# Performance work log

Measured on AMD Instinct MI355X. Metric: run time of the kernel, lower is better.

The kernel has to match this reference:

```python
import jax, jax.numpy as jnp
import numpy as np

K_NEIGHBORS = 16


def knn_idx(x, k):
    # x: (bs, n, 3) -> (bs, n, k) indices of k nearest points (incl. self)
    sq = jnp.sum(x * x, axis=-1)                      # (bs, n)
    inner = jnp.einsum('bnd,bmd->bnm', x, x)          # (bs, n, n)
    dist = sq[:, :, None] - 2.0 * inner + sq[:, None, :]
    _, idx = jax.lax.top_k(-dist, k)
    return idx


def gather_neighbors(feat, idx):
    # feat: (bs, n, d), idx: (bs, n, k) -> (bs, n, k, d)
    bs = feat.shape[0]
    return feat[jnp.arange(bs)[:, None, None], idx]


def setup_inputs() -> dict:
    key = jax.random.key(0)
    ks = jax.random.split(key, 20)
    bs, n, emb, inner, ph, ah = 4, 2048, 128, 128, 64, 4 * 128
    s = lambda k, sh, fan: jax.random.normal(k, sh, jnp.float32) * (1.0 / np.sqrt(fan))
    return {
        'query': jax.random.normal(ks[0], (bs, n, emb), jnp.float32),
        'key': jax.random.normal(ks[1], (bs, n, emb), jnp.float32),
        'value': jax.random.normal(ks[2], (bs, n, emb), jnp.float32),
        'canonical': jax.random.normal(ks[3], (bs, n, 3), jnp.float32),
        'wq': s(ks[4], (emb, inner), emb),
        'wk': s(ks[5], (emb, inner), emb),
        'wv': s(ks[6], (emb, inner), emb),
        'wo': s(ks[7], (inner, emb), inner),
        'bo': jnp.zeros((emb,), jnp.float32),
        'p1': s(ks[8], (3, ph), 3),
        'pb1': jnp.zeros((ph,), jnp.float32),
        'p2': s(ks[9], (ph, inner), ph),
        'pb2': jnp.zeros((inner,), jnp.float32),
        'a1': s(ks[10], (inner, ah), inner),
        'ab1': jnp.zeros((ah,), jnp.float32),
        'a2': s(ks[11], (ah, inner), ah),
        'ab2': jnp.zeros((inner,), jnp.float32),
    }


def reference(query, key, value, canonical, wq, wk, wv, wo, bo,
              p1, pb1, p2, pb2, a1, ab1, a2, ab2):
    k_nb = K_NEIGHBORS
    q = query @ wq                                    # (bs, n, d)
    k = key @ wk
    v = value @ wv
    idx = knn_idx(canonical, k_nb)                    # (bs, n, k)

    pos_nn = gather_neighbors(canonical, idx)         # (bs, n, k, 3)
    rel_pos = pos_nn - canonical[:, :, None, :]
    rel_pos_emb = jax.nn.relu(rel_pos @ p1 + pb1) @ p2 + pb2  # (bs, n, k, d)

    q_nn = gather_neighbors(q, idx)
    k_nn = gather_neighbors(k, idx)
    v_nn = gather_neighbors(v, idx) + rel_pos_emb

    sim = jax.nn.relu((q_nn - k_nn + rel_pos_emb) @ a1 + ab1) @ a2 + ab2
    attn = jax.nn.softmax(sim, axis=-1)               # softmax over feature dim
    norm = jnp.maximum(jnp.linalg.norm(attn, axis=-2, keepdims=True), 1e-12)
    attn = attn / norm                                # L2-normalize over neighbors

    agg = jnp.einsum('bijd,bijd->bid', attn, v_nn)    # (bs, n, d)
    return agg @ wo + bo
```

## Files before the change

kernel.cpp:

```cpp
#include <hip/hip_runtime.h>
#include <stdint.h>

typedef unsigned short u16;
typedef unsigned int u32;
typedef unsigned long long u64;
typedef __attribute__((ext_vector_type(8))) short short8;
typedef __attribute__((ext_vector_type(4))) float f32x4;

#define BSZ 4
#define NPT 2048
#define EMB 128
#define PH  64
#define AH  512
#define KNB 16

__device__ __forceinline__ u16 f2bf(float f) {
  union { float f; u32 u; } v; v.f = f;
  u32 r = (v.u >> 16) & 1u;
  v.u += 0x7fffu + r;
  return (u16)(v.u >> 16);
}
__device__ __forceinline__ float bf2f(u16 x) {
  union { u32 u; float f; } v; v.u = ((u32)x) << 16; return v.f;
}

__global__ __launch_bounds__(256) void k_transpose(
    const float* wq, const float* wk, const float* wv, const float* p2,
    const float* a1, const float* a2, const float* wo,
    u16* wqT, u16* wkT, u16* wvT, u16* p2T, u16* a1T, u16* a2T, u16* woT) {
  const float* src; u16* dst; int K, Nn;
  switch (blockIdx.x) {
    case 0: src = wq; dst = wqT; K = 128; Nn = 128; break;
    case 1: src = wk; dst = wkT; K = 128; Nn = 128; break;
    case 2: src = wv; dst = wvT; K = 128; Nn = 128; break;
    case 3: src = p2; dst = p2T; K = 64;  Nn = 128; break;
    case 4: src = a1; dst = a1T; K = 128; Nn = 512; break;
    case 5: src = a2; dst = a2T; K = 512; Nn = 128; break;
    default: src = wo; dst = woT; K = 128; Nn = 128; break;
  }
  for (int n = threadIdx.x; n < Nn; n += 256) {
    for (int k0 = 0; k0 < K; k0 += 8) {
      short8 vv;
      #pragma unroll
      for (int t = 0; t < 8; ++t)
        vv[t] = (short)f2bf(src[(k0 + t) * Nn + n]);
      *(short8*)(dst + n * K + k0) = vv;
    }
  }
}

__device__ __forceinline__ u32 f2sort(float f) {
  union { float f; u32 u; } v; v.f = f;
  return v.u ^ ((v.u >> 31) ? 0xFFFFFFFFu : 0x80000000u);
}

__global__ __launch_bounds__(256) void k_knn(const float* __restrict__ can,
                                             int* __restrict__ idx_out) {
  __shared__ float dists[4][NPT];
  int b = blockIdx.x >> 8;
  int qblk = blockIdx.x & 255;
  const float* cb = can + (size_t)b * NPT * 3;
  int wave = threadIdx.x >> 6, lane = threadIdx.x & 63;
  float* dw = dists[wave];
  #pragma unroll 1
  for (int t = 0; t < 2; ++t) {
    int i = qblk * 8 + wave * 2 + t;
    float xi = cb[i * 3 + 0], yi = cb[i * 3 + 1], zi = cb[i * 3 + 2];
    float sqi = __fadd_rn(__fadd_rn(__fmul_rn(xi, xi), __fmul_rn(yi, yi)),
                          __fmul_rn(zi, zi));
    u64 lmin = ~0ull;
    #pragma unroll 4
    for (int c = 0; c < NPT / 64; ++c) {
      int j = c * 64 + lane;
      const float* pj = cb + j * 3;
      float xj = pj[0], yj = pj[1], zj = pj[2];
      float sqj = __fadd_rn(__fadd_rn(__fmul_rn(xj, xj), __fmul_rn(yj, yj)),
                            __fmul_rn(zj, zj));
      float nn = __fadd_rn(__fadd_rn(__fmul_rn(xi, xj), __fmul_rn(yi, yj)),
                           __fmul_rn(zi, zj));
      float dist = __fadd_rn(__fsub_rn(sqi, __fmul_rn(2.0f, nn)), sqj);
      dw[j] = dist;
      u64 key = (((u64)f2sort(dist)) << 32) | (u32)j;
      lmin = key < lmin ? key : lmin;
    }
    #pragma unroll 1
    for (int r = 0; r < KNB; ++r) {
      u64 g = lmin;
      #pragma unroll
      for (int off = 32; off > 0; off >>= 1) {
        u64 o = __shfl_xor(g, off);
        g = o < g ? o : g;
      }
      int jw = (int)(u32)(g & 0xffffffffull);
      if (lane == 0) idx_out[((size_t)b * NPT + i) * KNB + r] = jw;
      if ((jw & 63) == lane) {
        union { u32 u; float f; } inf; inf.u = 0x7f800000u;
        dw[jw] = inf.f;
        lmin = ~0ull;
        #pragma unroll
        for (int c = 0; c < NPT / 64; ++c) {
          int j = c * 64 + lane;
          u64 key = (((u64)f2sort(dw[j])) << 32) | (u32)j;
          lmin = key < lmin ? key : lmin;
        }
      }
    }
  }
}

__device__ __forceinline__ void qkv_gemm(const u16* At, const u16* wT,
                                         int colbase, int fm, int quad,
                                         f32x4 acc[2][4]) {
  #pragma unroll
  for (int tn = 0; tn < 2; ++tn)
    #pragma unroll
    for (int tm = 0; tm < 4; ++tm) acc[tn][tm] = (f32x4){0.f, 0.f, 0.f, 0.f};
  #pragma unroll
  for (int ks = 0; ks < 4; ++ks) {
    int k0 = ks * 32 + quad * 8;
    short8 bfr0 = *(const short8*)(wT + (colbase + fm) * 128 + k0);
    short8 bfr1 = *(const short8*)(wT + (colbase + 16 + fm) * 128 + k0);
    #pragma unroll
    for (int tm = 0; tm < 4; ++tm) {
      short8 afr = *(const short8*)(At + (tm * 16 + fm) * 136 + k0);
      acc[0][tm] = __builtin_amdgcn_mfma_f32_16x16x32_bf16(afr, bfr0, acc[0][tm], 0, 0, 0);
      acc[1][tm] = __builtin_amdgcn_mfma_f32_16x16x32_bf16(afr, bfr1, acc[1][tm], 0, 0, 0);
    }
  }
}

__device__ __forceinline__ void qkv_stage(u16* At, const float* src, int rbase, int tid) {
  #pragma unroll
  for (int rep = 0; rep < 4; ++rep) {
    int linear = tid + 256 * rep;
    int row = linear >> 4;
    int c16 = linear & 15;
    const float* sp = src + (size_t)(rbase + row) * 128 + c16 * 8;
    f32x4 a = *(const f32x4*)(sp);
    f32x4 b = *(const f32x4*)(sp + 4);
    short8 vv;
    vv[0] = (short)f2bf(a[0]); vv[1] = (short)f2bf(a[1]);
    vv[2] = (short)f2bf(a[2]); vv[3] = (short)f2bf(a[3]);
    vv[4] = (short)f2bf(b[0]); vv[5] = (short)f2bf(b[1]);
    vv[6] = (short)f2bf(b[2]); vv[7] = (short)f2bf(b[3]);
    *(short8*)(At + row * 136 + c16 * 8) = vv;
  }
}

__global__ __launch_bounds__(256) void k_qkv(
    const float* __restrict__ query, const float* __restrict__ key,
    const float* __restrict__ value,
    const u16* __restrict__ wqT, const u16* __restrict__ wkT,
    const u16* __restrict__ wvT,
    float* __restrict__ qk_out, float* __restrict__ v_out) {
  __shared__ __align__(16) u16 At[64 * 136];
  int tid = threadIdx.x;
  int rbase = blockIdx.x * 64;
  int lane = tid & 63, wave = tid >> 6;
  int fm = lane & 15, quad = lane >> 4;
  int colbase = wave * 32;
  f32x4 accq[2][4], acck[2][4];

  qkv_stage(At, query, rbase, tid);
  __syncthreads();
  qkv_gemm(At, wqT, colbase, fm, quad, accq);
  __syncthreads();
  qkv_stage(At, key, rbase, tid);
  __syncthreads();
  qkv_gemm(At, wkT, colbase, fm, quad, acck);
  #pragma unroll
  for (int tn = 0; tn < 2; ++tn) {
    int col = colbase + tn * 16 + fm;
    #pragma unroll
    for (int tm = 0; tm < 4; ++tm)
      #pragma unroll
      for (int r = 0; r < 4; ++r) {
        int row = tm * 16 + quad * 4 + r;
        qk_out[(size_t)(rbase + row) * 128 + col] =
            accq[tn][tm][r] - acck[tn][tm][r];
      }
  }
  __syncthreads();
  qkv_stage(At, value, rbase, tid);
  __syncthreads();
  qkv_gemm(At, wvT, colbase, fm, quad, accq);
  #pragma unroll
  for (int tn = 0; tn < 2; ++tn) {
    int col = colbase + tn * 16 + fm;
    #pragma unroll
    for (int tm = 0; tm < 4; ++tm)
      #pragma unroll
      for (int r = 0; r < 4; ++r) {
        int row = tm * 16 + quad * 4 + r;
        v_out[(size_t)(rbase + row) * 128 + col] = accq[tn][tm][r];
      }
  }
}

#define XT_LD 136

__global__ __launch_bounds__(256, 3) void k_attn(
    const float* __restrict__ can,
    const float* __restrict__ qk_g, const float* __restrict__ v_g,
    const int* __restrict__ idx_g,
    const float* __restrict__ p1, const float* __restrict__ pb1,
    const u16* __restrict__ p2T, const float* __restrict__ pb2,
    const u16* __restrict__ a1T, const float* __restrict__ ab1,
    const u16* __restrict__ a2T, const float* __restrict__ ab2,
    const u16* __restrict__ woT, const float* __restrict__ bo,
    float* __restrict__ out) {
  __shared__ __align__(16) char smem[39168];
  u16* Xt = (u16*)(smem);
  u16* Hs = (u16*)(smem + 17408);
  u16* R1 = (u16*)(smem + 17408);
  float* Red1 = (float*)(smem + 34816);
  float* Red2 = (float*)(smem + 35840);
  float* Agg = (float*)(smem + 36864);
  int* Idx = (int*)(smem + 38912);

  const int b = blockIdx.x >> 9;
  const int qbase = (blockIdx.x & 511) * 4;
  const int tid = threadIdx.x;
  const int lane = tid & 63, wave = tid >> 6;
  const int fm = lane & 15, quad = lane >> 4;
  const int colbase = wave * 32;

  if (tid < 64) Idx[tid] = idx_g[((size_t)b * NPT + qbase) * KNB + tid];
  __syncthreads();

  {
    int row = tid >> 2, part = tid & 3;
    int j = Idx[row];
    int qi = qbase + (row >> 4);
    const float* cb = can + (size_t)b * NPT * 3;
    float r0 = cb[j * 3 + 0] - cb[qi * 3 + 0];
    float r1 = cb[j * 3 + 1] - cb[qi * 3 + 1];
    float r2 = cb[j * 3 + 2] - cb[qi * 3 + 2];
    #pragma unroll
    for (int hp = 0; hp < 8; ++hp) {
      int cp = part + 4 * hp;
      u32 pack = 0;
      #pragma unroll
      for (int e = 0; e < 2; ++e) {
        int hh = cp * 2 + e;
        float s = r0 * p1[hh];
        s = fmaf(r1, p1[PH + hh], s);
        s = fmaf(r2, p1[2 * PH + hh], s);
        s += pb1[hh];
        s = fmaxf(s, 0.0f);
        pack |= ((u32)f2bf(s)) << (16 * e);
      }
      *(u32*)(R1 + row * 72 + cp * 2) = pack;
    }
  }
  __syncthreads();

  u32 vp[4][4];
  {
    f32x4 acc[2][4];
    #pragma unroll
    for (int tn = 0; tn < 2; ++tn)
      #pragma unroll
      for (int tm = 0; tm < 4; ++tm) acc[tn][tm] = (f32x4){0.f, 0.f, 0.f, 0.f};
    #pragma unroll
    for (int ks = 0; ks < 2; ++ks) {
      int k0 = ks * 32 + quad * 8;
      short8 bfr0 = *(const short8*)(p2T + (colbase + fm) * PH + k0);
      short8 bfr1 = *(const short8*)(p2T + (colbase + 16 + fm) * PH + k0);
      #pragma unroll
      for (int tm = 0; tm < 4; ++tm) {
        short8 afr = *(const short8*)(R1 + (tm * 16 + fm) * 72 + k0);
        acc[0][tm] = __builtin_amdgcn_mfma_f32_16x16x32_bf16(afr, bfr0, acc[0][tm], 0, 0, 0);
        acc[1][tm] = __builtin_amdgcn_mfma_f32_16x16x32_bf16(afr, bfr1, acc[1][tm], 0, 0, 0);
      }
    }
    #pragma unroll
    for (int tn = 0; tn < 2; ++tn) {
      int col = colbase + tn * 16 + fm;
      float pb2c = pb2[col];
      #pragma unroll
      for (int tm = 0; tm < 4; ++tm)
        #pragma unroll
        for (int r = 0; r < 4; ++r) {
          int row = tm * 16 + quad * 4 + r;
          int j = Idx[row];
          float rpe = acc[tn][tm][r] + pb2c;
          size_t base = ((size_t)b * NPT + j) * EMB + col;
          Xt[row * XT_LD + col] = f2bf(qk_g[base] + rpe);
          u32 vb = (u32)f2bf(v_g[base] + rpe);
          if (tn == 0) vp[tm][r] = vb; else vp[tm][r] |= vb << 16;
        }
    }
  }
  __syncthreads();

  f32x4 accS[2][4];
  #pragma unroll
  for (int tn = 0; tn < 2; ++tn)
    #pragma unroll
    for (int tm = 0; tm < 4; ++tm) accS[tn][tm] = (f32x4){0.f, 0.f, 0.f, 0.f};
  #pragma unroll 1
  for (int c = 0; c < 4; ++c) {
    f32x4 acc1[2][4];
    #pragma unroll
    for (int tn = 0; tn < 2; ++tn)
      #pragma unroll
      for (int tm = 0; tm < 4; ++tm) acc1[tn][tm] = (f32x4){0.f, 0.f, 0.f, 0.f};
    #pragma unroll
    for (int ks = 0; ks < 4; ++ks) {
      int k0 = ks * 32 + quad * 8;
      short8 bfr0 = *(const short8*)(a1T + (c * 128 + colbase + fm) * 128 + k0);
      short8 bfr1 = *(const short8*)(a1T + (c * 128 + colbase + 16 + fm) * 128 + k0);
      #pragma unroll
      for (int tm = 0; tm < 4; ++tm) {
        short8 afr = *(const short8*)(Xt + (tm * 16 + fm) * XT_LD + k0);
        acc1[0][tm] = __builtin_amdgcn_mfma_f32_16x16x32_bf16(afr, bfr0, acc1[0][tm], 0, 0, 0);
        acc1[1][tm] = __builtin_amdgcn_mfma_f32_16x16x32_bf16(afr, bfr1, acc1[1][tm], 0, 0, 0);
      }
    }
    #pragma unroll
    for (int tn = 0; tn < 2; ++tn) {
      int lcol = colbase + tn * 16 + fm;
      float ab1c = ab1[c * 128 + lcol];
      #pragma unroll
      for (int tm = 0; tm < 4; ++tm)
        #pragma unroll
        for (int r = 0; r < 4; ++r) {
          int row = tm * 16 + quad * 4 + r;
          Hs[row * XT_LD + lcol] = f2bf(fmaxf(acc1[tn][tm][r] + ab1c, 0.0f));
        }
    }
    __syncthreads();
    #pragma unroll
    for (int ks = 0; ks < 4; ++ks) {
      int k0 = ks * 32 + quad * 8;
      short8 bfr0 = *(const short8*)(a2T + (colbase + fm) * AH + c * 128 + k0);
      short8 bfr1 = *(const short8*)(a2T + (colbase + 16 + fm) * AH + c * 128 + k0);
      #pragma unroll
      for (int tm = 0; tm < 4; ++tm) {
        short8 afr = *(const short8*)(Hs + (tm * 16 + fm) * XT_LD + k0);
        accS[0][tm] = __builtin_amdgcn_mfma_f32_16x16x32_bf16(afr, bfr0, accS[0][tm], 0, 0, 0);
        accS[1][tm] = __builtin_amdgcn_mfma_f32_16x16x32_bf16(afr, bfr1, accS[1][tm], 0, 0, 0);
      }
    }
    __syncthreads();
  }

  {
    float ab2c0 = ab2[colbase + fm];
    float ab2c1 = ab2[colbase + 16 + fm];
    float rm[4][4];
    #pragma unroll
    for (int tm = 0; tm < 4; ++tm)
      #pragma unroll
      for (int r = 0; r < 4; ++r) {
        accS[0][tm][r] += ab2c0;
        accS[1][tm][r] += ab2c1;
        rm[tm][r] = fmaxf(accS[0][tm][r], accS[1][tm][r]);
      }
    #pragma unroll
    for (int off = 1; off <= 8; off <<= 1)
      #pragma unroll
      for (int tm = 0; tm < 4; ++tm)
        #pragma unroll
        for (int r = 0; r < 4; ++r)
          rm[tm][r] = fmaxf(rm[tm][r], __shfl_xor(rm[tm][r], off));
    if (fm == 0) {
      #pragma unroll
      for (int tm = 0; tm < 4; ++tm)
        #pragma unroll
        for (int r = 0; r < 4; ++r)
          Red1[wave * 64 + tm * 16 + quad * 4 + r] = rm[tm][r];
    }
    __syncthreads();
    #pragma unroll
    for (int tm = 0; tm < 4; ++tm)
      #pragma unroll
      for (int r = 0; r < 4; ++r) {
        int row = tm * 16 + quad * 4 + r;
        float m = fmaxf(fmaxf(Red1[row], Red1[64 + row]),
                        fmaxf(Red1[128 + row], Red1[192 + row]));
        float e0 = __expf(accS[0][tm][r] - m);
        float e1 = __expf(accS[1][tm][r] - m);
        accS[0][tm][r] = e0;
        accS[1][tm][r] = e1;
        rm[tm][r] = e0 + e1;
      }
    #pragma unroll
    for (int off = 1; off <= 8; off <<= 1)
      #pragma unroll
      for (int tm = 0; tm < 4; ++tm)
        #pragma unroll
        for (int r = 0; r < 4; ++r)
          rm[tm][r] += __shfl_xor(rm[tm][r], off);
    if (fm == 0) {
      #pragma unroll
      for (int tm = 0; tm < 4; ++tm)
        #pragma unroll
        for (int r = 0; r < 4; ++r)
          Red2[wave * 64 + tm * 16 + quad * 4 + r] = rm[tm][r];
    }
    __syncthreads();
    #pragma unroll
    for (int tm = 0; tm < 4; ++tm)
      #pragma unroll
      for (int r = 0; r < 4; ++r) {
        int row = tm * 16 + quad * 4 + r;
        float sum = (Red2[row] + Red2[64 + row]) +
                    (Red2[128 + row] + Red2[192 + row]);
        float inv = 1.0f / sum;
        accS[0][tm][r] *= inv;
        accS[1][tm][r] *= inv;
      }
  }

  #pragma unroll
  for (int tn = 0; tn < 2; ++tn)
    #pragma unroll
    for (int tm = 0; tm < 4; ++tm) {
      float ssq = 0.f, wav = 0.f;
      #pragma unroll
      for (int r = 0; r < 4; ++r) {
        float a = accS[tn][tm][r];
        u16 vb = (u16)(tn == 0 ? (vp[tm][r] & 0xffffu) : (vp[tm][r] >> 16));
        ssq = fmaf(a, a, ssq);
        wav = fmaf(a, bf2f(vb), wav);
      }
      ssq += __shfl_xor(ssq, 16); ssq += __shfl_xor(ssq, 32);
      wav += __shfl_xor(wav, 16); wav += __shfl_xor(wav, 32);
      if (quad == 0)
        Agg[tm * EMB + colbase + tn * 16 + fm] =
            wav / fmaxf(sqrtf(ssq), 1e-12f);
    }
  __syncthreads();

  {
    int d = tid & 127, qp = tid >> 7;
    float boc = bo[d];
    #pragma unroll
    for (int qi2 = 0; qi2 < 2; ++qi2) {
      int q = qp * 2 + qi2;
      float o = 0.f;
      #pragma unroll
      for (int k8 = 0; k8 < 16; ++k8) {
        short8 w8 = *(const short8*)(woT + d * 128 + k8 * 8);
        #pragma unroll
        for (int e = 0; e < 8; ++e)
          o = fmaf(Agg[q * EMB + k8 * 8 + e], bf2f((u16)w8[e]), o);
      }
      out[((size_t)b * NPT + qbase + q) * EMB + d] = o + boc;
    }
  }
}

extern "C" void kernel_launch(void* const* d_in, const int* in_sizes, int n_in,
                              void* d_out, int out_size, void* d_ws, size_t ws_size,
                              hipStream_t stream) {
  (void)in_sizes; (void)n_in; (void)out_size; (void)ws_size;
  const float* query = (const float*)d_in[0];
  const float* key_i = (const float*)d_in[1];
  const float* value = (const float*)d_in[2];
  const float* can   = (const float*)d_in[3];
  const float* wq  = (const float*)d_in[4];
  const float* wk  = (const float*)d_in[5];
  const float* wv  = (const float*)d_in[6];
  const float* wo  = (const float*)d_in[7];
  const float* bo  = (const float*)d_in[8];
  const float* p1  = (const float*)d_in[9];
  const float* pb1 = (const float*)d_in[10];
  const float* p2  = (const float*)d_in[11];
  const float* pb2 = (const float*)d_in[12];
  const float* a1  = (const float*)d_in[13];
  const float* ab1 = (const float*)d_in[14];
  const float* a2  = (const float*)d_in[15];
  const float* ab2 = (const float*)d_in[16];

  char* ws = (char*)d_ws;
  float* qk_ws = (float*)(ws + 0);
  float* v_ws  = (float*)(ws + 4194304);
  int* idx_ws  = (int*)(ws + 8388608);
  u16* wqT = (u16*)(ws + 8912896);
  u16* wkT = (u16*)(ws + 8945664);
  u16* wvT = (u16*)(ws + 8978432);
  u16* p2T = (u16*)(ws + 9011200);
  u16* a1T = (u16*)(ws + 9027584);
  u16* a2T = (u16*)(ws + 9158656);
  u16* woT = (u16*)(ws + 9289728);
  float* out = (float*)d_out;

  k_transpose<<<dim3(7), dim3(256), 0, stream>>>(
      wq, wk, wv, p2, a1, a2, wo, wqT, wkT, wvT, p2T, a1T, a2T, woT);
  k_knn<<<dim3(1024), dim3(256), 0, stream>>>(can, idx_ws);
  k_qkv<<<dim3(128), dim3(256), 0, stream>>>(
      query, key_i, value, wqT, wkT, wvT, qk_ws, v_ws);
  k_attn<<<dim3(2048), dim3(256), 0, stream>>>(
      can, qk_ws, v_ws, idx_ws, p1, pb1, p2T, pb2, a1T, ab1, a2T, ab2,
      woT, bo, out);
}
```

Before: 315.1 us.

## Pack q-k and v as interleaved bf16 pairs and prefetch neighbor gathers

New measurement: 319.1 us. About the same (+1.3%).

```diff
diff --git a/kernel.cpp b/kernel.cpp
--- a/kernel.cpp
+++ b/kernel.cpp
@@ -152,7 +152,7 @@
     const float* __restrict__ value,
     const u16* __restrict__ wqT, const u16* __restrict__ wkT,
     const u16* __restrict__ wvT,
-    float* __restrict__ qk_out, float* __restrict__ v_out) {
+    u32* __restrict__ pv_out) {
   __shared__ __align__(16) u16 At[64 * 136];
   int tid = threadIdx.x;
   int rbase = blockIdx.x * 64;
@@ -168,6 +168,17 @@
   qkv_stage(At, key, rbase, tid);
   __syncthreads();
   qkv_gemm(At, wkT, colbase, fm, quad, acck);
+  u32 qk2[4][4];
+  #pragma unroll
+  for (int tm = 0; tm < 4; ++tm)
+    #pragma unroll
+    for (int r = 0; r < 4; ++r)
+      qk2[tm][r] = (u32)f2bf(accq[0][tm][r] - acck[0][tm][r]) |
+                   (((u32)f2bf(accq[1][tm][r] - acck[1][tm][r])) << 16);
+  __syncthreads();
+  qkv_stage(At, value, rbase, tid);
+  __syncthreads();
+  qkv_gemm(At, wvT, colbase, fm, quad, accq);
   #pragma unroll
   for (int tn = 0; tn < 2; ++tn) {
     int col = colbase + tn * 16 + fm;
@@ -176,23 +187,9 @@
       #pragma unroll
       for (int r = 0; r < 4; ++r) {
         int row = tm * 16 + quad * 4 + r;
-        qk_out[(size_t)(rbase + row) * 128 + col] =
-            accq[tn][tm][r] - acck[tn][tm][r];
-      }
-  }
-  __syncthreads();
-  qkv_stage(At, value, rbase, tid);
-  __syncthreads();
-  qkv_gemm(At, wvT, colbase, fm, quad, accq);
-  #pragma unroll
-  for (int tn = 0; tn < 2; ++tn) {
-    int col = colbase + tn * 16 + fm;
-    #pragma unroll
-    for (int tm = 0; tm < 4; ++tm)
-      #pragma unroll
-      for (int r = 0; r < 4; ++r) {
-        int row = tm * 16 + quad * 4 + r;
-        v_out[(size_t)(rbase + row) * 128 + col] = accq[tn][tm][r];
+        u32 qkb = tn == 0 ? (qk2[tm][r] & 0xffffu) : (qk2[tm][r] >> 16);
+        u32 pack = qkb | (((u32)f2bf(accq[tn][tm][r])) << 16);
+        pv_out[(size_t)(rbase + row) * 128 + col] = pack;
       }
   }
 }
@@ -201,7 +198,7 @@
 
 __global__ __launch_bounds__(256, 3) void k_attn(
     const float* __restrict__ can,
-    const float* __restrict__ qk_g, const float* __restrict__ v_g,
+    const u32* __restrict__ pv_g,
     const int* __restrict__ idx_g,
     const float* __restrict__ p1, const float* __restrict__ pb1,
     const u16* __restrict__ p2T, const float* __restrict__ pb2,
@@ -228,6 +225,20 @@
   if (tid < 64) Idx[tid] = idx_g[((size_t)b * NPT + qbase) * KNB + tid];
   __syncthreads();
 
+  u32 pvld[2][4][4];
+  #pragma unroll
+  for (int tn = 0; tn < 2; ++tn) {
+    int col = colbase + tn * 16 + fm;
+    #pragma unroll
+    for (int tm = 0; tm < 4; ++tm)
+      #pragma unroll
+      for (int r = 0; r < 4; ++r) {
+        int row = tm * 16 + quad * 4 + r;
+        int j = Idx[row];
+        pvld[tn][tm][r] = pv_g[((size_t)b * NPT + j) * EMB + col];
+      }
+  }
+
   {
     int row = tid >> 2, part = tid & 3;
     int j = Idx[row];
@@ -283,11 +294,10 @@
         #pragma unroll
         for (int r = 0; r < 4; ++r) {
           int row = tm * 16 + quad * 4 + r;
-          int j = Idx[row];
           float rpe = acc[tn][tm][r] + pb2c;
-          size_t base = ((size_t)b * NPT + j) * EMB + col;
-          Xt[row * XT_LD + col] = f2bf(qk_g[base] + rpe);
-          u32 vb = (u32)f2bf(v_g[base] + rpe);
+          u32 w = pvld[tn][tm][r];
+          Xt[row * XT_LD + col] = f2bf(bf2f((u16)(w & 0xffffu)) + rpe);
+          u32 vb = (u32)f2bf(bf2f((u16)(w >> 16)) + rpe);
           if (tn == 0) vp[tm][r] = vb; else vp[tm][r] |= vb << 16;
         }
     }
@@ -476,8 +486,7 @@
   const float* ab2 = (const float*)d_in[16];
 
   char* ws = (char*)d_ws;
-  float* qk_ws = (float*)(ws + 0);
-  float* v_ws  = (float*)(ws + 4194304);
+  u32* pv_ws = (u32*)(ws + 0);
   int* idx_ws  = (int*)(ws + 8388608);
   u16* wqT = (u16*)(ws + 8912896);
   u16* wkT = (u16*)(ws + 8945664);
@@ -492,8 +501,8 @@
       wq, wk, wv, p2, a1, a2, wo, wqT, wkT, wvT, p2T, a1T, a2T, woT);
   k_knn<<<dim3(1024), dim3(256), 0, stream>>>(can, idx_ws);
   k_qkv<<<dim3(128), dim3(256), 0, stream>>>(
-      query, key_i, value, wqT, wkT, wvT, qk_ws, v_ws);
+      query, key_i, value, wqT, wkT, wvT, pv_ws);
   k_attn<<<dim3(2048), dim3(256), 0, stream>>>(
-      can, qk_ws, v_ws, idx_ws, p1, pb1, p2T, pb2, a1T, ab1, a2T, ab2,
+      can, pv_ws, idx_ws, p1, pb1, p2T, pb2, a1T, ab1, a2T, ab2,
       woT, bo, out);
 }
```
